# Kernel optimization log

Measured on AMD Instinct MI355X. Metric: run time of the kernel, lower is better.

Reference implementation:

```python
import jax, jax.numpy as jnp
import numpy as np

N = 500_000
D_IN, D_HID, NUM_HEADS, D_OUT = 256, 128, 4, 4


def setup_inputs() -> dict:
    key = jax.random.key(0)
    k1, k2, k3, k4 = jax.random.split(key, 4)
    x = jax.random.normal(k1, (N, D_IN), dtype=jnp.float32)
    W1 = jax.random.normal(k2, (D_IN, D_HID), dtype=jnp.float32)
    W2 = jax.random.normal(k3, (D_HID, D_OUT), dtype=jnp.float32)
    heads = jax.random.randint(k4, (N,), 0, NUM_HEADS, dtype=jnp.int32)
    return {"x": x, "W1": W1, "W2": W2, "heads": heads}


def reference(x, W1, W2, heads):
    # linear_1: e3nn Linear over pure-scalar irreps == dense matmul with
    # path normalization 1/sqrt(fan_in)
    h = (x @ W1) * (1.0 / np.sqrt(D_IN))          # [N, D_HID]
    # gated nonlinearity (scalars only -> plain activation)
    h = jax.nn.silu(h)
    # mask_head: channels grouped into NUM_HEADS blocks of D_HID//NUM_HEADS;
    # keep only the block matching each node's head
    hb = h.reshape(N, NUM_HEADS, D_HID // NUM_HEADS)
    onehot = jax.nn.one_hot(heads, NUM_HEADS, dtype=h.dtype)  # [N, H]
    h = (hb * onehot[:, :, None]).reshape(N, D_HID)
    # linear_2
    return (h @ W2) * (1.0 / np.sqrt(D_HID))      # [N, D_OUT]
```

## Files before the change

### kernel.cpp

```cpp
#include <hip/hip_runtime.h>
#include <hip/hip_bf16.h>


#define D_IN   256
#define TILE_M 128

typedef __attribute__((ext_vector_type(8))) short  short8;
typedef __attribute__((ext_vector_type(4))) float  float4v;
typedef __attribute__((ext_vector_type(4))) int    int4v;

__device__ __forceinline__ unsigned short f2bf_rne(float f) {
    union { float f; unsigned int u; } cv; cv.f = f;
    unsigned int u = cv.u;
    return (unsigned short)((u + 0x7FFFu + ((u >> 16) & 1u)) >> 16);
}

__device__ __forceinline__ short8 pack8(float4v lo, float4v hi) {
    short8 r;
    r[0] = (short)f2bf_rne(lo[0]); r[1] = (short)f2bf_rne(lo[1]);
    r[2] = (short)f2bf_rne(lo[2]); r[3] = (short)f2bf_rne(lo[3]);
    r[4] = (short)f2bf_rne(hi[0]); r[5] = (short)f2bf_rne(hi[1]);
    r[6] = (short)f2bf_rne(hi[2]); r[7] = (short)f2bf_rne(hi[3]);
    return r;
}

__global__ void prep_w1(const float* __restrict__ W1, unsigned short* __restrict__ W1p) {
    int idx = blockIdx.x * 256 + threadIdx.x;
    int i = idx >> 7;
    int j = idx & 127;
    unsigned short b = f2bf_rne(W1[idx] * 0.0625f);
    int kt = i >> 5, q = (i >> 3) & 3, jj = i & 7;
    int nt = j >> 4, mm = j & 15;
    int lane = q * 16 + mm;
    W1p[(((kt * 8 + nt) * 64 + lane) << 3) + jj] = b;
}

__global__ __launch_bounds__(256)
void readout_v2(const float* __restrict__ x,
                const unsigned short* __restrict__ W1p,
                const float* __restrict__ W2,
                const int* __restrict__ heads,
                float* __restrict__ out, int nrows) {
    const int t    = threadIdx.x;
    const int w    = t >> 6;
    const int lane = t & 63;
    const int q    = lane >> 4;
    const int m    = lane & 15;
    const int rowbase = blockIdx.x * TILE_M + w * 32;

    const int r0 = min(rowbase + m,      nrows - 1);
    const int r1 = min(rowbase + 16 + m, nrows - 1);
    const float* xr0 = x + (size_t)r0 * D_IN + q * 8;
    const float* xr1 = x + (size_t)r1 * D_IN + q * 8;
    const unsigned short* bbase = W1p + lane * 8;

    float4v acc[2][8];
    #pragma unroll
    for (int rt = 0; rt < 2; ++rt)
        #pragma unroll
        for (int nt = 0; nt < 8; ++nt) acc[rt][nt] = (float4v){0.f, 0.f, 0.f, 0.f};

    #pragma unroll
    for (int kt = 0; kt < 8; ++kt) {
        float4v a0lo = *(const float4v*)(xr0 + kt * 32);
        float4v a0hi = *(const float4v*)(xr0 + kt * 32 + 4);
        float4v a1lo = *(const float4v*)(xr1 + kt * 32);
        float4v a1hi = *(const float4v*)(xr1 + kt * 32 + 4);
        short8 b[8];
        #pragma unroll
        for (int nt = 0; nt < 8; ++nt)
            b[nt] = *(const short8*)(bbase + (kt * 8 + nt) * 512);
        short8 a0 = pack8(a0lo, a0hi);
        short8 a1 = pack8(a1lo, a1hi);
        #pragma unroll
        for (int nt = 0; nt < 8; ++nt) {
            acc[0][nt] = __builtin_amdgcn_mfma_f32_16x16x32_bf16(a0, b[nt], acc[0][nt], 0, 0, 0);
            acc[1][nt] = __builtin_amdgcn_mfma_f32_16x16x32_bf16(a1, b[nt], acc[1][nt], 0, 0, 0);
        }
    }

    const float sc = 0.08838834764831845f;
    const bool full = (rowbase + 32) <= nrows;
    #pragma unroll
    for (int rt = 0; rt < 2; ++rt) {
        int4v hv;
        if (full) {
            hv = *(const int4v*)(heads + rowbase + rt * 16 + q * 4);
        } else {
            #pragma unroll
            for (int e = 0; e < 4; ++e)
                hv[e] = heads[min(rowbase + rt * 16 + q * 4 + e, nrows - 1)];
        }
        #pragma unroll
        for (int reg = 0; reg < 4; ++reg) {
            int h = hv[reg];
            float v0 = (h == 0) ? acc[rt][0][reg] : (h == 1) ? acc[rt][2][reg]
                     : (h == 2) ? acc[rt][4][reg] : acc[rt][6][reg];
            float v1 = (h == 0) ? acc[rt][1][reg] : (h == 1) ? acc[rt][3][reg]
                     : (h == 2) ? acc[rt][5][reg] : acc[rt][7][reg];
            float s0 = v0 / (1.0f + __expf(-v0));
            float s1 = v1 / (1.0f + __expf(-v1));
            float4v w2a = *(const float4v*)(W2 + (h * 32 + m) * 4);
            float4v w2b = *(const float4v*)(W2 + (h * 32 + 16 + m) * 4);
            float4v o = w2a * s0 + w2b * s1;
            #pragma unroll
            for (int d = 1; d < 16; d <<= 1) {
                o[0] += __shfl_xor(o[0], d, 64);
                o[1] += __shfl_xor(o[1], d, 64);
                o[2] += __shfl_xor(o[2], d, 64);
                o[3] += __shfl_xor(o[3], d, 64);
            }
            if (m == 0) {
                int gr = rowbase + rt * 16 + q * 4 + reg;
                if (gr < nrows) {
                    float4v res = { o[0] * sc, o[1] * sc, o[2] * sc, o[3] * sc };
                    *(float4v*)(out + (size_t)gr * 4) = res;
                }
            }
        }
    }
}

extern "C" void kernel_launch(void* const* d_in, const int* in_sizes, int n_in,
                              void* d_out, int out_size, void* d_ws, size_t ws_size,
                              hipStream_t stream) {
    const float* x     = (const float*)d_in[0];
    const float* W1    = (const float*)d_in[1];
    const float* W2    = (const float*)d_in[2];
    const int*   heads = (const int*)d_in[3];
    float*       out   = (float*)d_out;
    unsigned short* W1p = (unsigned short*)d_ws;

    int nrows = in_sizes[0] / D_IN;

    prep_w1<<<128, 256, 0, stream>>>(W1, W1p);
    int nb = (nrows + TILE_M - 1) / TILE_M;
    readout_v2<<<nb, 256, 0, stream>>>(x, W1p, W2, heads, out, nrows);
}
```

Baseline: 710.8 us.

## Stage packed W1 tiles in shared memory, swap bf16 conversion intrinsic

Each block now cooperatively copies the packed bf16 W1 into LDS in two 32 KB halves. All four waves then read B fragments from LDS instead of each wave fetching them from global/L2. The float-to-bf16 packing also switches from a hand-written rounding routine to the library __float2bfloat16 intrinsic. This adds two block-wide barriers per block and 32 KB of LDS, which can limit occupancy, and the x loads are not overlapped with the staging.

New measurement: 686.9 us. 3.4% less time.

```diff
diff --git a/kernel.cpp b/kernel.cpp
--- a/kernel.cpp
+++ b/kernel.cpp
@@ -17,10 +17,14 @@
 
 __device__ __forceinline__ short8 pack8(float4v lo, float4v hi) {
     short8 r;
-    r[0] = (short)f2bf_rne(lo[0]); r[1] = (short)f2bf_rne(lo[1]);
-    r[2] = (short)f2bf_rne(lo[2]); r[3] = (short)f2bf_rne(lo[3]);
-    r[4] = (short)f2bf_rne(hi[0]); r[5] = (short)f2bf_rne(hi[1]);
-    r[6] = (short)f2bf_rne(hi[2]); r[7] = (short)f2bf_rne(hi[3]);
+    r[0] = (short)__bfloat16_as_ushort(__float2bfloat16(lo[0]));
+    r[1] = (short)__bfloat16_as_ushort(__float2bfloat16(lo[1]));
+    r[2] = (short)__bfloat16_as_ushort(__float2bfloat16(lo[2]));
+    r[3] = (short)__bfloat16_as_ushort(__float2bfloat16(lo[3]));
+    r[4] = (short)__bfloat16_as_ushort(__float2bfloat16(hi[0]));
+    r[5] = (short)__bfloat16_as_ushort(__float2bfloat16(hi[1]));
+    r[6] = (short)__bfloat16_as_ushort(__float2bfloat16(hi[2]));
+    r[7] = (short)__bfloat16_as_ushort(__float2bfloat16(hi[3]));
     return r;
 }
 
@@ -36,11 +40,13 @@
 }
 
 __global__ __launch_bounds__(256)
-void readout_v2(const float* __restrict__ x,
+void readout_v4(const float* __restrict__ x,
                 const unsigned short* __restrict__ W1p,
                 const float* __restrict__ W2,
                 const int* __restrict__ heads,
                 float* __restrict__ out, int nrows) {
+    __shared__ unsigned short sB[16384];
+
     const int t    = threadIdx.x;
     const int w    = t >> 6;
     const int lane = t & 63;
@@ -52,7 +58,7 @@
     const int r1 = min(rowbase + 16 + m, nrows - 1);
     const float* xr0 = x + (size_t)r0 * D_IN + q * 8;
     const float* xr1 = x + (size_t)r1 * D_IN + q * 8;
-    const unsigned short* bbase = W1p + lane * 8;
+    const unsigned short* sbase = sB + lane * 8;
 
     float4v acc[2][8];
     #pragma unroll
@@ -61,21 +67,38 @@
         for (int nt = 0; nt < 8; ++nt) acc[rt][nt] = (float4v){0.f, 0.f, 0.f, 0.f};
 
     #pragma unroll
-    for (int kt = 0; kt < 8; ++kt) {
-        float4v a0lo = *(const float4v*)(xr0 + kt * 32);
-        float4v a0hi = *(const float4v*)(xr0 + kt * 32 + 4);
-        float4v a1lo = *(const float4v*)(xr1 + kt * 32);
-        float4v a1hi = *(const float4v*)(xr1 + kt * 32 + 4);
-        short8 b[8];
+    for (int p = 0; p < 2; ++p) {
+        if (p) __syncthreads();
+        {
+            const unsigned short* gsrc = W1p + p * 16384 + t * 8;
+            float4v v[8];
+            #pragma unroll
+            for (int i = 0; i < 8; ++i)
+                v[i] = *(const float4v*)(gsrc + i * 2048);
+            #pragma unroll
+            for (int i = 0; i < 8; ++i)
+                *(float4v*)(sB + t * 8 + i * 2048) = v[i];
+        }
+        __syncthreads();
+
         #pragma unroll
-        for (int nt = 0; nt < 8; ++nt)
-            b[nt] = *(const short8*)(bbase + (kt * 8 + nt) * 512);
-        short8 a0 = pack8(a0lo, a0hi);
-        short8 a1 = pack8(a1lo, a1hi);
-        #pragma unroll
-        for (int nt = 0; nt < 8; ++nt) {
-            acc[0][nt] = __builtin_amdgcn_mfma_f32_16x16x32_bf16(a0, b[nt], acc[0][nt], 0, 0, 0);
-            acc[1][nt] = __builtin_amdgcn_mfma_f32_16x16x32_bf16(a1, b[nt], acc[1][nt], 0, 0, 0);
+        for (int ktl = 0; ktl < 4; ++ktl) {
+            const int kt = p * 4 + ktl;
+            float4v a0lo = *(const float4v*)(xr0 + kt * 32);
+            float4v a0hi = *(const float4v*)(xr0 + kt * 32 + 4);
+            float4v a1lo = *(const float4v*)(xr1 + kt * 32);
+            float4v a1hi = *(const float4v*)(xr1 + kt * 32 + 4);
+            short8 b[8];
+            #pragma unroll
+            for (int nt = 0; nt < 8; ++nt)
+                b[nt] = *(const short8*)(sbase + (ktl * 8 + nt) * 512);
+            short8 a0 = pack8(a0lo, a0hi);
+            short8 a1 = pack8(a1lo, a1hi);
+            #pragma unroll
+            for (int nt = 0; nt < 8; ++nt) {
+                acc[0][nt] = __builtin_amdgcn_mfma_f32_16x16x32_bf16(a0, b[nt], acc[0][nt], 0, 0, 0);
+                acc[1][nt] = __builtin_amdgcn_mfma_f32_16x16x32_bf16(a1, b[nt], acc[1][nt], 0, 0, 0);
+            }
         }
     }
 
@@ -135,5 +158,5 @@
 
     prep_w1<<<128, 256, 0, stream>>>(W1, W1p);
     int nb = (nrows + TILE_M - 1) / TILE_M;
-    readout_v2<<<nb, 256, 0, stream>>>(x, W1p, W2, heads, out, nrows);
+    readout_v4<<<nb, 256, 0, stream>>>(x, W1p, W2, heads, out, nrows);
 }
```
